# Optimization experiments

Measured on AMD Instinct MI355X. Metric: run time of the kernel, lower is better.

Reference implementation:

```python
import jax, jax.numpy as jnp
import numpy as np

N, E, D, H, C, L = 50000, 600000, 128, 128, 64, 3
LN_EPS = 1e-5


def setup_inputs() -> dict:
    key = jax.random.key(0)
    ks = jax.random.split(key, 6)
    x = jax.random.normal(ks[0], (N, D), jnp.float32)
    edge_index = jax.random.randint(ks[1], (2, E), 0, N, jnp.int32)
    Wg = jax.random.normal(ks[2], (L, D, H), jnp.float32) * (1.0 / np.sqrt(D))
    bg = jnp.zeros((L, H), jnp.float32)
    ln_g = jnp.ones((L, H), jnp.float32)
    ln_b = jnp.zeros((L, H), jnp.float32)
    mlp_W1 = jax.random.normal(ks[3], (D + L * H, H), jnp.float32) * (1.0 / np.sqrt(D + L * H))
    mlp_b1 = jnp.zeros((H,), jnp.float32)
    mlp_W2 = jax.random.normal(ks[4], (H, C), jnp.float32) * (1.0 / np.sqrt(H))
    mlp_b2 = jnp.zeros((C,), jnp.float32)
    return {"x": x, "edge_index": edge_index, "Wg": Wg, "bg": bg,
            "ln_g": ln_g, "ln_b": ln_b, "mlp_W1": mlp_W1, "mlp_b1": mlp_b1,
            "mlp_W2": mlp_W2, "mlp_b2": mlp_b2}


def _layer_norm(h, g, b):
    mu = jnp.mean(h, axis=-1, keepdims=True)
    var = jnp.mean((h - mu) ** 2, axis=-1, keepdims=True)
    return g * (h - mu) * jax.lax.rsqrt(var + LN_EPS) + b


def _gcn(h, W, b, src, dst, dinv):
    # GCNConv with added self-loops and symmetric normalization:
    # out = D^{-1/2} (A + I) D^{-1/2} (h W) + b
    hW = h @ W                                   # [N, H]
    coef = (dinv[src] * dinv[dst])[:, None]      # [E, 1]
    agg = jax.ops.segment_sum(hW[src] * coef, dst, num_segments=N)
    agg = agg + hW * (dinv * dinv)[:, None]      # self-loop term
    return agg + b


def reference(x, edge_index, Wg, bg, ln_g, ln_b, mlp_W1, mlp_b1, mlp_W2, mlp_b2):
    src, dst = edge_index[0], edge_index[1]
    # degree including self-loop
    deg = jnp.ones((N,), x.dtype).at[dst].add(1.0)
    dinv = jax.lax.rsqrt(deg)
    feats = [x]
    h = x
    for i in range(L):  # small fixed layer count
        h = _gcn(h, Wg[i], bg[i], src, dst, dinv)
        h = _layer_norm(h, ln_g[i], ln_b[i])
        h = jax.nn.relu(h)
        feats.append(h)
    xc = jnp.concatenate(feats, axis=1)          # [N, D + L*H]
    z = jax.nn.relu(xc @ mlp_W1 + mlp_b1)
    z = z @ mlp_W2 + mlp_b2
    return jax.nn.softmax(z, axis=1)
```

## Files before the change

### kernel.cpp

```cpp
#include <hip/hip_runtime.h>
#include <math.h>

#define D 128
#define HH 128
#define CC 64
#define NLAYERS 3
#define LN_EPS 1e-5f

typedef __attribute__((ext_vector_type(8))) short bf16x8;
typedef __attribute__((ext_vector_type(4))) float f32x4;
typedef unsigned short u16;
typedef unsigned int u32;

__device__ __forceinline__ u16 f2bf(float f) {
    u32 u = __float_as_uint(f);
    u32 r = u + 0x7FFFu + ((u >> 16) & 1u);
    return (u16)(r >> 16);
}
__device__ __forceinline__ float bf2f(u16 h) {
    return __uint_as_float(((u32)h) << 16);
}

__global__ void k_prep(const float* __restrict__ x, u16* __restrict__ xh,
                       const float* __restrict__ Wg, u16* __restrict__ WgtH,
                       const float* __restrict__ W1, u16* __restrict__ W1tH,
                       const float* __restrict__ W2, u16* __restrict__ W2tH,
                       u16* __restrict__ W2tL,
                       const int* __restrict__ dst, int* __restrict__ cnt,
                       int N, int E)
{
    int i = blockIdx.x * blockDim.x + threadIdx.x;
    int nx4 = N * (D / 4);
    if (i < nx4) {
        float4 v = *(const float4*)(x + (size_t)i * 4);
        int row = i >> 5, c = (i & 31) << 2;
        ushort4 o;
        o.x = f2bf(v.x); o.y = f2bf(v.y); o.z = f2bf(v.z); o.w = f2bf(v.w);
        *(ushort4*)&xh[(size_t)row * 512 + c] = o;
        return;
    }
    i -= nx4;
    if (i < NLAYERS * D * HH) {
        int k = i >> 7, n = i & 127;
        int kc = k >> 5, q = (k >> 3) & 3, j = k & 7;
        WgtH[(((kc * 4 + q) << 7) + n) * 8 + j] = f2bf(Wg[i]);
        return;
    }
    i -= NLAYERS * D * HH;
    if (i < (D + NLAYERS * HH) * HH) {
        int k = i >> 7, n = i & 127;
        int kc = k >> 5, q = (k >> 3) & 3, j = k & 7;
        W1tH[(((kc * 4 + q) << 7) + n) * 8 + j] = f2bf(W1[i]);
        return;
    }
    i -= (D + NLAYERS * HH) * HH;
    if (i < HH * CC) {
        int k = i >> 6, n = i & 63;
        int kc = k >> 5, q = (k >> 3) & 3, j = k & 7;
        float v = W2[i];
        u16 h = f2bf(v);
        int o = (((kc * 4 + q) << 6) + n) * 8 + j;
        W2tH[o] = h;
        W2tL[o] = f2bf(v - bf2f(h));
        return;
    }
    i -= HH * CC;
    if (i < E) atomicAdd(&cnt[dst[i]], 1);
}


__global__ void k_scan_a(const int* __restrict__ cnt, int* __restrict__ rowptr,
                         int* __restrict__ bsum, int N) {
    __shared__ int ws[16];
    int tid  = threadIdx.x;
    int lane = tid & 63, wv = tid >> 6;
    int i = blockIdx.x * 1024 + tid;
    int v = (i < N) ? cnt[i] : 0;
    int incl = v;
    #pragma unroll
    for (int off = 1; off < 64; off <<= 1) {
        int u = __shfl_up(incl, off, 64);
        if (lane >= off) incl += u;
    }
    if (lane == 63) ws[wv] = incl;
    __syncthreads();
    if (wv == 0) {
        int s = (lane < 16) ? ws[lane] : 0;
        #pragma unroll
        for (int off = 1; off < 16; off <<= 1) {
            int u = __shfl_up(s, off, 64);
            if (lane >= off) s += u;
        }
        if (lane < 16) ws[lane] = s;
    }
    __syncthreads();
    int add = (wv == 0) ? 0 : ws[wv - 1];
    if (i < N) rowptr[i] = add + incl - v;
    if (tid == 1023) bsum[blockIdx.x] = ws[15];
}

__global__ void k_scan_c(int* __restrict__ rowptr, const int* __restrict__ bsum,
                         const int* __restrict__ cnt, float* __restrict__ dinv,
                         int* __restrict__ cursor, int N, int E, int nsb) {
    __shared__ int sb[64];
    if (threadIdx.x < 64) {
        int t = threadIdx.x;
        int v = (t < nsb) ? bsum[t] : 0;
        int incl = v;
        #pragma unroll
        for (int off = 1; off < 64; off <<= 1) {
            int u = __shfl_up(incl, off, 64);
            if (t >= off) incl += u;
        }
        sb[t] = incl - v;
    }
    __syncthreads();
    int i = blockIdx.x * blockDim.x + threadIdx.x;
    if (i < N) {
        int v = rowptr[i] + sb[i >> 10];
        rowptr[i] = v;
        cursor[i] = v;
        dinv[i] = rsqrtf(1.0f + (float)cnt[i]);
    }
    if (i == 0) rowptr[N] = E;
}

__global__ void k_scatter(const int* __restrict__ src, const int* __restrict__ dst,
                          const float* __restrict__ dinv,
                          int* __restrict__ cursor, int2* __restrict__ ecol, int E) {
    int i = blockIdx.x * blockDim.x + threadIdx.x;
    if (i < E) {
        int s = src[i], d = dst[i];
        int p = atomicAdd(&cursor[d], 1);
        float c = dinv[s] * dinv[d];
        ecol[p] = make_int2(s, __float_as_int(c));
    }
}

__global__ __launch_bounds__(256) void k_gemm_lf(
    const u16* __restrict__ A, int colOff,
    const u16* __restrict__ Bt, u16* __restrict__ OUTb, int N)
{
    const int tid  = threadIdx.x;
    const int lane = tid & 63;
    const int wave = tid >> 6;
    const int wr   = wave & 1;
    const int wc   = wave >> 1;
    const int quad = lane >> 4;
    const int l15  = lane & 15;
    const int row0 = blockIdx.x * 64;

    const u16* pA[2];
    #pragma unroll
    for (int i = 0; i < 2; ++i) {
        int r = row0 + wr * 32 + i * 16 + l15;
        if (r >= N) r = N - 1;
        pA[i] = A + (size_t)r * 512 + colOff + quad * 8;
    }
    const u16* pB = Bt + ((size_t)quad * 128 + wc * 64 + l15) * 8;

    bf16x8 ah[4][2], bh[4][4];
    #pragma unroll
    for (int kc = 0; kc < 4; ++kc) {
        #pragma unroll
        for (int i = 0; i < 2; ++i)
            ah[kc][i] = *(const bf16x8*)(pA[i] + kc * 32);
        #pragma unroll
        for (int j = 0; j < 4; ++j)
            bh[kc][j] = *(const bf16x8*)(pB + (size_t)kc * 4096 + j * 128);
    }

    f32x4 acc[2][4];
    #pragma unroll
    for (int i = 0; i < 2; ++i)
        #pragma unroll
        for (int j = 0; j < 4; ++j)
            #pragma unroll
            for (int r = 0; r < 4; ++r) acc[i][j][r] = 0.f;

    #pragma unroll
    for (int kc = 0; kc < 4; ++kc)
        #pragma unroll
        for (int i = 0; i < 2; ++i)
            #pragma unroll
            for (int j = 0; j < 4; ++j)
                acc[i][j] = __builtin_amdgcn_mfma_f32_16x16x32_bf16(ah[kc][i], bh[kc][j], acc[i][j], 0, 0, 0);

    #pragma unroll
    for (int i = 0; i < 2; ++i)
        #pragma unroll
        for (int j = 0; j < 4; ++j) {
            int col = wc * 64 + j * 16 + l15;
            #pragma unroll
            for (int r = 0; r < 4; ++r) {
                int grow = row0 + wr * 32 + i * 16 + quad * 4 + r;
                if (grow < N)
                    OUTb[(size_t)grow * 128 + col] = f2bf(acc[i][j][r]);
            }
        }
}

__global__ __launch_bounds__(256) void k_mlp_fused(
    const u16* __restrict__ xcH,
    const u16* __restrict__ B1t, const float* __restrict__ b1,
    const u16* __restrict__ W2h, const u16* __restrict__ W2l,
    const float* __restrict__ b2, float* __restrict__ out, int N)
{
    __shared__ u16 sZh[64 * 128];
    __shared__ u16 sZl[64 * 128];

    const int tid  = threadIdx.x;
    const int lane = tid & 63;
    const int wave = tid >> 6;
    const int wr   = wave & 1;
    const int wc   = wave >> 1;
    const int quad = lane >> 4;
    const int l15  = lane & 15;
    const int row0 = blockIdx.x * 64;

    const u16* pA[2];
    #pragma unroll
    for (int i = 0; i < 2; ++i) {
        int r = row0 + wr * 32 + i * 16 + l15;
        if (r >= N) r = N - 1;
        pA[i] = xcH + (size_t)r * 512 + quad * 8;
    }
    const u16* pB = B1t + ((size_t)quad * 128 + wc * 64 + l15) * 8;

    f32x4 acc[2][4];
    #pragma unroll
    for (int i = 0; i < 2; ++i)
        #pragma unroll
        for (int j = 0; j < 4; ++j)
            #pragma unroll
            for (int r = 0; r < 4; ++r) acc[i][j][r] = 0.f;

    #pragma unroll
    for (int kp = 0; kp < 4; ++kp) {
        bf16x8 ah[4][2], bh[4][4];
        #pragma unroll
        for (int c = 0; c < 4; ++c) {
            const int g = kp * 4 + c;
            #pragma unroll
            for (int i = 0; i < 2; ++i)
                ah[c][i] = *(const bf16x8*)(pA[i] + g * 32);
            #pragma unroll
            for (int j = 0; j < 4; ++j)
                bh[c][j] = *(const bf16x8*)(pB + (size_t)g * 4096 + j * 128);
        }
        #pragma unroll
        for (int c = 0; c < 4; ++c)
            #pragma unroll
            for (int i = 0; i < 2; ++i)
                #pragma unroll
                for (int j = 0; j < 4; ++j)
                    acc[i][j] = __builtin_amdgcn_mfma_f32_16x16x32_bf16(
                        ah[c][i], bh[c][j], acc[i][j], 0, 0, 0);
    }

    #pragma unroll
    for (int jt = 0; jt < 4; ++jt) {
        int col = wc * 64 + jt * 16 + l15;
        float bv = b1[col];
        int qq = col >> 3, jj = col & 7;
        #pragma unroll
        for (int i = 0; i < 2; ++i) {
            #pragma unroll
            for (int rr = 0; rr < 4; ++rr) {
                int row = wr * 32 + i * 16 + quad * 4 + rr;
                float v = fmaxf(acc[i][jt][rr] + bv, 0.f);
                u16 h = f2bf(v);
                sZh[(qq * 64 + row) * 8 + jj] = h;
                sZl[(qq * 64 + row) * 8 + jj] = f2bf(v - bf2f(h));
            }
        }
    }
    __syncthreads();

    {
        f32x4 oacc[4];
        #pragma unroll
        for (int j = 0; j < 4; ++j)
            #pragma unroll
            for (int r = 0; r < 4; ++r) oacc[j][r] = 0.f;

        #pragma unroll
        for (int kc = 0; kc < 4; ++kc) {
            int qq = kc * 4 + quad;
            bf16x8 zh = *(const bf16x8*)&sZh[(qq * 64 + wave * 16 + l15) * 8];
            bf16x8 zl = *(const bf16x8*)&sZl[(qq * 64 + wave * 16 + l15) * 8];
            #pragma unroll
            for (int jt = 0; jt < 4; ++jt) {
                int n = jt * 16 + l15;
                bf16x8 wh = *(const bf16x8*)&W2h[(qq * 64 + n) * 8];
                bf16x8 wl = *(const bf16x8*)&W2l[(qq * 64 + n) * 8];
                oacc[jt] = __builtin_amdgcn_mfma_f32_16x16x32_bf16(zh, wh, oacc[jt], 0, 0, 0);
                oacc[jt] = __builtin_amdgcn_mfma_f32_16x16x32_bf16(zh, wl, oacc[jt], 0, 0, 0);
                oacc[jt] = __builtin_amdgcn_mfma_f32_16x16x32_bf16(zl, wh, oacc[jt], 0, 0, 0);
            }
        }

        #pragma unroll
        for (int jt = 0; jt < 4; ++jt) {
            float bv = b2[jt * 16 + l15];
            #pragma unroll
            for (int r = 0; r < 4; ++r) oacc[jt][r] += bv;
        }
        #pragma unroll
        for (int r = 0; r < 4; ++r) {
            float m = fmaxf(fmaxf(oacc[0][r], oacc[1][r]), fmaxf(oacc[2][r], oacc[3][r]));
            #pragma unroll
            for (int mask = 8; mask; mask >>= 1) m = fmaxf(m, __shfl_xor(m, mask, 64));
            float p0 = __expf(oacc[0][r] - m);
            float p1 = __expf(oacc[1][r] - m);
            float p2 = __expf(oacc[2][r] - m);
            float p3 = __expf(oacc[3][r] - m);
            float s = p0 + p1 + p2 + p3;
            #pragma unroll
            for (int mask = 8; mask; mask >>= 1) s += __shfl_xor(s, mask, 64);
            float inv = 1.0f / s;
            int grow = row0 + wave * 16 + quad * 4 + r;
            if (grow < N) {
                float* o = out + (size_t)grow * CC + l15;
                o[0]  = p0 * inv;
                o[16] = p1 * inv;
                o[32] = p2 * inv;
                o[48] = p3 * inv;
            }
        }
    }
}

__global__ __launch_bounds__(256, 8) void k_agg_ln(
    const u16* __restrict__ hWb,
    const int* __restrict__ rowptr, const int2* __restrict__ ecol,
    const float* __restrict__ dinv,
    const float* __restrict__ bg, const float* __restrict__ g,
    const float* __restrict__ b,
    u16* __restrict__ outHi, int N)
{
    const int lane = threadIdx.x & 63;
    const int c0   = (lane & 31) << 2;

    const float4 bgv = *(const float4*)(bg + c0);
    const float4 gv  = *(const float4*)(g + c0);
    const float4 bv  = *(const float4*)(b + c0);

    const int nslots = gridDim.x * 8;
    for (int wid = blockIdx.x * 8 + ((threadIdx.x >> 6) << 1) + (lane >> 5);
         wid < N; wid += nslots) {
        float di = dinv[wid];
        float sc = di * di;

        uint2 hv = *(const uint2*)(hWb + (size_t)wid * HH + c0);
        float a0 = bf2f((u16)hv.x) * sc;
        float a1 = bf2f((u16)(hv.x >> 16)) * sc;
        float a2 = bf2f((u16)hv.y) * sc;
        float a3 = bf2f((u16)(hv.y >> 16)) * sc;
        float q0 = 0.f, q1 = 0.f, q2 = 0.f, q3 = 0.f;

        int e0 = rowptr[wid];
        int m  = rowptr[wid + 1] - e0;
        const int2* ep = ecol + e0;

        int k = 0;
        for (; k + 4 <= m; k += 4) {
            int2 p[4];
            uint2 v[4];
            #pragma unroll
            for (int t = 0; t < 4; ++t) p[t] = ep[k + t];
            #pragma unroll
            for (int t = 0; t < 4; ++t)
                v[t] = *(const uint2*)(hWb + (size_t)p[t].x * HH + c0);
            #pragma unroll
            for (int t = 0; t < 4; ++t) {
                float c = __int_as_float(p[t].y);
                float x0 = bf2f((u16)v[t].x) * c;
                float x1 = bf2f((u16)(v[t].x >> 16)) * c;
                float x2 = bf2f((u16)v[t].y) * c;
                float x3 = bf2f((u16)(v[t].y >> 16)) * c;
                if (t & 1) { q0 += x0; q1 += x1; q2 += x2; q3 += x3; }
                else       { a0 += x0; a1 += x1; a2 += x2; a3 += x3; }
            }
        }
        if (k < m) {
            int2 p0 = ep[k];
            int2 p1 = (k + 1 < m) ? ep[k + 1] : p0;
            int2 p2 = (k + 2 < m) ? ep[k + 2] : p0;
            uint2 v0 = *(const uint2*)(hWb + (size_t)p0.x * HH + c0);
            uint2 v1 = *(const uint2*)(hWb + (size_t)p1.x * HH + c0);
            uint2 v2 = *(const uint2*)(hWb + (size_t)p2.x * HH + c0);
            float cc0 = __int_as_float(p0.y);
            float cc1 = (k + 1 < m) ? __int_as_float(p1.y) : 0.f;
            float cc2 = (k + 2 < m) ? __int_as_float(p2.y) : 0.f;
            a0 += bf2f((u16)v0.x) * cc0;  a1 += bf2f((u16)(v0.x >> 16)) * cc0;
            a2 += bf2f((u16)v0.y) * cc0;  a3 += bf2f((u16)(v0.y >> 16)) * cc0;
            q0 += bf2f((u16)v1.x) * cc1;  q1 += bf2f((u16)(v1.x >> 16)) * cc1;
            q2 += bf2f((u16)v1.y) * cc1;  q3 += bf2f((u16)(v1.y >> 16)) * cc1;
            a0 += bf2f((u16)v2.x) * cc2;  a1 += bf2f((u16)(v2.x >> 16)) * cc2;
            a2 += bf2f((u16)v2.y) * cc2;  a3 += bf2f((u16)(v2.y >> 16)) * cc2;
        }
        a0 += q0; a1 += q1; a2 += q2; a3 += q3;
        a0 += bgv.x; a1 += bgv.y; a2 += bgv.z; a3 += bgv.w;

        float ssum = (a0 + a1) + (a2 + a3);
        #pragma unroll
        for (int off = 16; off; off >>= 1) ssum += __shfl_xor(ssum, off, 64);
        float mu = ssum * (1.0f / 128.0f);
        float d0 = a0 - mu, d1 = a1 - mu, d2 = a2 - mu, d3 = a3 - mu;
        float vsum = (d0 * d0 + d1 * d1) + (d2 * d2 + d3 * d3);
        #pragma unroll
        for (int off = 16; off; off >>= 1) vsum += __shfl_xor(vsum, off, 64);
        float rstd = rsqrtf(vsum * (1.0f / 128.0f) + LN_EPS);

        float o0 = fmaxf(gv.x * d0 * rstd + bv.x, 0.f);
        float o1 = fmaxf(gv.y * d1 * rstd + bv.y, 0.f);
        float o2 = fmaxf(gv.z * d2 * rstd + bv.z, 0.f);
        float o3 = fmaxf(gv.w * d3 * rstd + bv.w, 0.f);
        uint2 o;
        o.x = (u32)f2bf(o0) | ((u32)f2bf(o1) << 16);
        o.y = (u32)f2bf(o2) | ((u32)f2bf(o3) << 16);
        *(uint2*)&outHi[(size_t)wid * 512 + c0] = o;
    }
}

extern "C" void kernel_launch(void* const* d_in, const int* in_sizes, int n_in,
                              void* d_out, int out_size, void* d_ws, size_t ws_size,
                              hipStream_t stream) {
    const float* x   = (const float*)d_in[0];
    const int*   ei  = (const int*)  d_in[1];
    const float* Wg  = (const float*)d_in[2];
    const float* bg  = (const float*)d_in[3];
    const float* lng = (const float*)d_in[4];
    const float* lnb = (const float*)d_in[5];
    const float* W1  = (const float*)d_in[6];
    const float* b1  = (const float*)d_in[7];
    const float* W2  = (const float*)d_in[8];
    const float* b2  = (const float*)d_in[9];
    float* out = (float*)d_out;

    const int N = in_sizes[0] / D;
    const int E = in_sizes[1] / 2;
    const int* srcp = ei;
    const int* dstp = ei + E;

    char* ws = (char*)d_ws;
    size_t off = 0;
    auto alloc = [&](size_t bytes) -> void* {
        void* p = ws + off;
        off += (bytes + 511) & ~(size_t)511;
        return p;
    };
    int*   cnt    = (int*)  alloc((size_t)N * 4);
    int*   rowptr = (int*)  alloc((size_t)(N + 1) * 4);
    int*   cursor = (int*)  alloc((size_t)N * 4);
    int*   bsum   = (int*)  alloc(64 * 4);
    int2*  ecol   = (int2*) alloc((size_t)E * 8);
    float* dinv   = (float*)alloc((size_t)N * 4);
    u16*   hWb    = (u16*)  alloc((size_t)N * HH * 2);
    u16*   xcH    = (u16*)  alloc((size_t)N * 512 * 2);
    u16*   WgtH   = (u16*)  alloc((size_t)NLAYERS * D * HH * 2);
    u16*   W1tH   = (u16*)  alloc((size_t)(D + NLAYERS * HH) * HH * 2);
    u16*   W2tH   = (u16*)  alloc((size_t)HH * CC * 2);
    u16*   W2tL   = (u16*)  alloc((size_t)HH * CC * 2);

    const int B = 256;
    const int gE = (E + B - 1) / B;
    const int nsb = (N + 1023) / 1024;

    hipMemsetAsync(cnt, 0, (size_t)N * 4, stream);

    const int prepTotal = N * (D / 4) + NLAYERS * D * HH
                        + (D + NLAYERS * HH) * HH + HH * CC + E;
    k_prep<<<(prepTotal + B - 1) / B, B, 0, stream>>>(x, xcH, Wg, WgtH, W1, W1tH,
                                                      W2, W2tH, W2tL, dstp, cnt, N, E);
    k_scan_a<<<nsb, 1024, 0, stream>>>(cnt, rowptr, bsum, N);
    k_scan_c<<<(N + B - 1) / B, B, 0, stream>>>(rowptr, bsum, cnt, dinv, cursor, N, E, nsb);
    k_scatter<<<gE, B, 0, stream>>>(srcp, dstp, dinv, cursor, ecol, E);

    const int gemmBlocks = (N + 63) / 64;
    const int mlpBlocks  = (N + 63) / 64;
    const int aggBlocks  = 2048;

    for (int l = 0; l < NLAYERS; ++l) {
        k_gemm_lf<<<gemmBlocks, B, 0, stream>>>(xcH, l * HH,
                                                WgtH + (size_t)l * D * HH, hWb, N);
        k_agg_ln<<<aggBlocks, B, 0, stream>>>(hWb, rowptr, ecol, dinv,
                                              bg + (size_t)l * HH,
                                              lng + (size_t)l * HH,
                                              lnb + (size_t)l * HH,
                                              xcH + (size_t)(l + 1) * HH, N);
    }

    k_mlp_fused<<<mlpBlocks, B, 0, stream>>>(xcH, W1tH, b1,
                                             W2tH, W2tL, b2, out, N);
}
```

Measured before the change: 311.7 us.

## Stage A tiles through LDS via direct global-to-LDS loads in GEMMs

Both the GCN linear GEMM and the fused MLP GEMM now load the 64-row A tile into shared memory with global_load_lds 16-byte transfers, using an XOR swizzle so the LDS reads that feed the MFMAs avoid bank conflicts. Each row of the tile is then fetched once per block and shared across the column waves, instead of every wave reading its A fragments straight from global memory. In exchange, the MLP kernel's k-loop gains two barriers per iteration and the kernels use more shared memory, which can reduce occupancy and serialize loads with compute.

New measurement: 294.0 us. 5.7% less time.

```diff
diff --git a/kernel.cpp b/kernel.cpp
--- a/kernel.cpp
+++ b/kernel.cpp
@@ -19,6 +19,12 @@
 }
 __device__ __forceinline__ float bf2f(u16 h) {
     return __uint_as_float(((u32)h) << 16);
+}
+
+__device__ __forceinline__ void gload_lds16(const void* g, void* l) {
+    __builtin_amdgcn_global_load_lds(
+        (const __attribute__((address_space(1))) void*)g,
+        (__attribute__((address_space(3))) void*)l, 16, 0, 0);
 }
 
 __global__ void k_prep(const float* __restrict__ x, u16* __restrict__ xh,
@@ -141,6 +147,8 @@
     const u16* __restrict__ A, int colOff,
     const u16* __restrict__ Bt, u16* __restrict__ OUTb, int N)
 {
+    __shared__ u16 sA[64 * 128];
+
     const int tid  = threadIdx.x;
     const int lane = tid & 63;
     const int wave = tid >> 6;
@@ -150,25 +158,35 @@
     const int l15  = lane & 15;
     const int row0 = blockIdx.x * 64;
 
-    const u16* pA[2];
-    #pragma unroll
-    for (int i = 0; i < 2; ++i) {
-        int r = row0 + wr * 32 + i * 16 + l15;
-        if (r >= N) r = N - 1;
-        pA[i] = A + (size_t)r * 512 + colOff + quad * 8;
-    }
+    #pragma unroll
+    for (int rd = 0; rd < 4; ++rd) {
+        int idx  = rd * 256 + tid;
+        int row  = idx >> 4;
+        int gp   = idx & 15;
+        int gs   = gp ^ (row & 7);
+        int grow = row0 + row; if (grow >= N) grow = N - 1;
+        const u16* src = A + (size_t)grow * 512 + colOff + gs * 8;
+        gload_lds16(src, &sA[(size_t)(rd * 256 + (tid & ~63)) * 8]);
+    }
+
     const u16* pB = Bt + ((size_t)quad * 128 + wc * 64 + l15) * 8;
-
-    bf16x8 ah[4][2], bh[4][4];
-    #pragma unroll
-    for (int kc = 0; kc < 4; ++kc) {
-        #pragma unroll
-        for (int i = 0; i < 2; ++i)
-            ah[kc][i] = *(const bf16x8*)(pA[i] + kc * 32);
+    bf16x8 bh[4][4];
+    #pragma unroll
+    for (int kc = 0; kc < 4; ++kc)
         #pragma unroll
         for (int j = 0; j < 4; ++j)
             bh[kc][j] = *(const bf16x8*)(pB + (size_t)kc * 4096 + j * 128);
-    }
+
+    __syncthreads();
+
+    const int rL[2] = { wr * 32 + l15, wr * 32 + 16 + l15 };
+    bf16x8 ah[4][2];
+    #pragma unroll
+    for (int kc = 0; kc < 4; ++kc)
+        #pragma unroll
+        for (int i = 0; i < 2; ++i)
+            ah[kc][i] = *(const bf16x8*)&sA[rL[i] * 128
+                           + (((kc << 2) | quad) ^ (rL[i] & 7)) * 8];
 
     f32x4 acc[2][4];
     #pragma unroll
@@ -206,6 +224,7 @@
     const u16* __restrict__ W2h, const u16* __restrict__ W2l,
     const float* __restrict__ b2, float* __restrict__ out, int N)
 {
+    __shared__ u16 sA[64 * 128];
     __shared__ u16 sZh[64 * 128];
     __shared__ u16 sZl[64 * 128];
 
@@ -218,14 +237,8 @@
     const int l15  = lane & 15;
     const int row0 = blockIdx.x * 64;
 
-    const u16* pA[2];
-    #pragma unroll
-    for (int i = 0; i < 2; ++i) {
-        int r = row0 + wr * 32 + i * 16 + l15;
-        if (r >= N) r = N - 1;
-        pA[i] = xcH + (size_t)r * 512 + quad * 8;
-    }
     const u16* pB = B1t + ((size_t)quad * 128 + wc * 64 + l15) * 8;
+    const int rL[2] = { wr * 32 + l15, wr * 32 + 16 + l15 };
 
     f32x4 acc[2][4];
     #pragma unroll
@@ -237,17 +250,33 @@
 
     #pragma unroll
     for (int kp = 0; kp < 4; ++kp) {
-        bf16x8 ah[4][2], bh[4][4];
-        #pragma unroll
-        for (int c = 0; c < 4; ++c) {
-            const int g = kp * 4 + c;
+        #pragma unroll
+        for (int rd = 0; rd < 4; ++rd) {
+            int idx  = rd * 256 + tid;
+            int row  = idx >> 4;
+            int gp   = idx & 15;
+            int gs   = gp ^ (row & 7);
+            int grow = row0 + row; if (grow >= N) grow = N - 1;
+            const u16* src = xcH + (size_t)grow * 512 + kp * 128 + gs * 8;
+            gload_lds16(src, &sA[(size_t)(rd * 256 + (tid & ~63)) * 8]);
+        }
+        bf16x8 bh[4][4];
+        #pragma unroll
+        for (int c = 0; c < 4; ++c)
+            #pragma unroll
+            for (int j = 0; j < 4; ++j)
+                bh[c][j] = *(const bf16x8*)(pB + (size_t)(kp * 4 + c) * 4096 + j * 128);
+
+        __syncthreads();
+
+        bf16x8 ah[4][2];
+        #pragma unroll
+        for (int c = 0; c < 4; ++c)
             #pragma unroll
             for (int i = 0; i < 2; ++i)
-                ah[c][i] = *(const bf16x8*)(pA[i] + g * 32);
-            #pragma unroll
-            for (int j = 0; j < 4; ++j)
-                bh[c][j] = *(const bf16x8*)(pB + (size_t)g * 4096 + j * 128);
-        }
+                ah[c][i] = *(const bf16x8*)&sA[rL[i] * 128
+                               + (((c << 2) | quad) ^ (rL[i] & 7)) * 8];
+
         #pragma unroll
         for (int c = 0; c < 4; ++c)
             #pragma unroll
@@ -256,6 +285,8 @@
                 for (int j = 0; j < 4; ++j)
                     acc[i][j] = __builtin_amdgcn_mfma_f32_16x16x32_bf16(
                         ah[c][i], bh[c][j], acc[i][j], 0, 0, 0);
+
+        __syncthreads();
     }
 
     #pragma unroll
```
